# Kernel tuning notes

Hardware: AMD Instinct MI355X
Metric: run time of the kernel (lower is better)

## Reference

```python
import jax, jax.numpy as jnp
import numpy as np

DIN, DK, DV, DR, NH, DMODEL = 512, 64, 64, 16, 8, 512
N = 4096
TOT = DK + DK + DV + DR  # per-head projection width = 208


def setup_inputs() -> dict:
    key = jax.random.key(0)
    k1, k2, k3, k4 = jax.random.split(key, 4)
    H = jax.random.normal(k1, (N, DIN), dtype=jnp.float32)
    D = jax.random.normal(k2, (N, N, DR), dtype=jnp.float32)
    attention_mask = jnp.zeros((N, N), dtype=jnp.float32)  # 0 = allowed
    # learned params (Linear, no bias): stored as [in, out] for x @ W
    W = jax.random.normal(k3, (DIN, NH * TOT), dtype=jnp.float32) / np.sqrt(DIN)
    Wout = jax.random.normal(k4, (NH * DV, DMODEL), dtype=jnp.float32) / np.sqrt(NH * DV)
    return {"H": H, "D": D, "attention_mask": attention_mask, "W": W, "Wout": Wout}


def reference(H, D, attention_mask, W, Wout):
    n = H.shape[0]
    # project and split into per-head Q, K, V, R: [h, n, *]
    H2 = (H @ W).reshape(n, NH, TOT).transpose(1, 0, 2)
    Q, K, V, R = jnp.split(H2, [DK, 2 * DK, 2 * DK + DV], axis=-1)
    # relative/route bias: RD[h,i,j] = sum_r R[h,i,r] * D[i,j,r]
    RD = jnp.einsum('hir,ijr->hij', R, D)
    scale = 1.0 / np.sqrt(DK + DR)
    scores = scale * (jnp.einsum('hid,hjd->hij', Q, K) + RD) + attention_mask
    probs = jax.nn.softmax(scores, axis=-1)
    ctx = jnp.einsum('hij,hjd->hid', probs, V)          # [h, n, dv]
    ctx = ctx.transpose(1, 0, 2).reshape(n, NH * DV)    # [n, h*dv]
    return ctx @ Wout                                    # [n, dmodel]
```

## Files before the change

kernel.cpp:

```cpp
#include <hip/hip_runtime.h>
#include <hip/hip_bf16.h>

#define NN 4096
#define NH 8
#define TOT 208
#define NPROJ 1664
#define BJ 32
#define NT (NN/BJ)

typedef __attribute__((ext_vector_type(8))) short short8;
typedef __attribute__((ext_vector_type(4))) short short4_t;
typedef __attribute__((ext_vector_type(4))) float float4_t;

#define MFMA __builtin_amdgcn_mfma_f32_16x16x32_bf16

__device__ __forceinline__ short f2bf(float f){
  union { float f; unsigned u; } v; v.f = f;
  unsigned r = v.u + 0x7fffu + ((v.u >> 16) & 1u);
  return (short)(r >> 16);
}

__device__ __forceinline__ short8 cvt8(float4_t a, float4_t b){
  union { short8 s; unsigned u[4]; } r;
  asm("v_cvt_pk_bf16_f32 %0, %1, %2" : "=v"(r.u[0]) : "v"(a[0]), "v"(a[1]));
  asm("v_cvt_pk_bf16_f32 %0, %1, %2" : "=v"(r.u[1]) : "v"(a[2]), "v"(a[3]));
  asm("v_cvt_pk_bf16_f32 %0, %1, %2" : "=v"(r.u[2]) : "v"(b[0]), "v"(b[1]));
  asm("v_cvt_pk_bf16_f32 %0, %1, %2" : "=v"(r.u[3]) : "v"(b[2]), "v"(b[3]));
  return r.s;
}

#define BAR() do{ \
    asm volatile("s_waitcnt lgkmcnt(0)" ::: "memory"); \
    __builtin_amdgcn_s_barrier(); \
    asm volatile("" ::: "memory"); \
  }while(0)

__global__ void k_cvt(const float* __restrict__ in, short* __restrict__ out, int n4){
  int i = blockIdx.x*256 + threadIdx.x;
  if(i >= n4) return;
  float4_t v = *(const float4_t*)(in + (size_t)i*4);
  short4_t o;
  o[0]=f2bf(v[0]); o[1]=f2bf(v[1]); o[2]=f2bf(v[2]); o[3]=f2bf(v[3]);
  *(short4_t*)(out + (size_t)i*4) = o;
}

__global__ void k_trans(const float* __restrict__ in, short* __restrict__ out, int R, int C){
  __shared__ float tile[32][33];
  int bc = blockIdx.x*32, br = blockIdx.y*32;
  int tx = threadIdx.x, ty = threadIdx.y;
  #pragma unroll
  for(int dy=0; dy<32; dy+=8){
    int r = br+ty+dy, c = bc+tx;
    if(r<R && c<C) tile[ty+dy][tx] = in[(size_t)r*C + c];
  }
  __syncthreads();
  #pragma unroll
  for(int dy=0; dy<32; dy+=8){
    int c = bc+ty+dy, r = br+tx;
    if(c<C && r<R) out[(size_t)c*R + r] = f2bf(tile[tx][ty+dy]);
  }
}

__global__ __launch_bounds__(256) void k_gemm(
    const short* __restrict__ A, const short* __restrict__ Bt, float* __restrict__ C,
    int M, int Ncols, int K)
{
  __shared__ __align__(16) short As[2][2048];
  __shared__ __align__(16) short Bs[2][2048];
  const int tid = threadIdx.x;
  const int l = tid & 63, w = tid >> 6;
  const int wm = w >> 1, wn = w & 1;
  const int g = l >> 4, i16 = l & 15;
  const size_t bm = (size_t)blockIdx.x * 64, bn = (size_t)blockIdx.y * 64;
  const int r = tid >> 2, cb = tid & 3;
  const int dst = r*32 + ((cb ^ (r&3))*8);
  const short* Ag = A + (bm + (size_t)r)*K + cb*8;
  const short* Bg = Bt + (bn + (size_t)r)*K + cb*8;
  float4_t z4 = {0.f,0.f,0.f,0.f};
  float4_t acc00=z4, acc01=z4, acc10=z4, acc11=z4;
  short8 ta = *(const short8*)(Ag);
  short8 tb = *(const short8*)(Bg);
  *(short8*)&As[0][dst] = ta;
  *(short8*)&Bs[0][dst] = tb;
  const int nk = K >> 5;
  int c = 0;
  const int swa = (g ^ (i16&3))*8;
  for(int kt=0; kt<nk; kt++){
    __syncthreads();
    if(kt+1 < nk){
      ta = *(const short8*)(Ag + (kt+1)*32);
      tb = *(const short8*)(Bg + (kt+1)*32);
    }
    short8 a0 = *(const short8*)&As[c][(wm*32 + i16)*32 + swa];
    short8 a1 = *(const short8*)&As[c][(wm*32 + 16 + i16)*32 + swa];
    short8 b0 = *(const short8*)&Bs[c][(wn*32 + i16)*32 + swa];
    short8 b1 = *(const short8*)&Bs[c][(wn*32 + 16 + i16)*32 + swa];
    acc00 = MFMA(a0,b0,acc00,0,0,0); acc01 = MFMA(a0,b1,acc01,0,0,0);
    acc10 = MFMA(a1,b0,acc10,0,0,0); acc11 = MFMA(a1,b1,acc11,0,0,0);
    if(kt+1 < nk){
      *(short8*)&As[c^1][dst] = ta;
      *(short8*)&Bs[c^1][dst] = tb;
    }
    c ^= 1;
  }
  #pragma unroll
  for(int rr=0; rr<4; rr++){
    C[(bm + wm*32 +      4*g + rr)*(size_t)Ncols + bn + wn*32 + i16]      = acc00[rr];
    C[(bm + wm*32 +      4*g + rr)*(size_t)Ncols + bn + wn*32 + 16 + i16] = acc01[rr];
    C[(bm + wm*32 + 16 + 4*g + rr)*(size_t)Ncols + bn + wn*32 + i16]      = acc10[rr];
    C[(bm + wm*32 + 16 + 4*g + rr)*(size_t)Ncols + bn + wn*32 + 16 + i16] = acc11[rr];
  }
}

__global__ void k_pack(const float* __restrict__ H2, short* __restrict__ Qp,
                       short* __restrict__ Kp, short* __restrict__ Vp, short* __restrict__ Rp){
  int T = blockIdx.x*256 + threadIdx.x;
  if(T < 262144){
    int l = T & 63; int rest = T >> 6;
    int kb = rest & 1; rest >>= 1;
    int it = rest & 255; int h = rest >> 8;
    int i = it*16 + (l & 15);
    int col = h*TOT + kb*32 + 8*(l>>4);
    const float* s = H2 + (size_t)i*NPROJ + col;
    short8 v;
    #pragma unroll
    for(int e=0;e<8;e++) v[e] = f2bf(s[e]);
    *(short8*)(Qp + (size_t)T*8) = v;
  } else if(T < 524288){
    int T2 = T - 262144;
    int l = T2 & 63; int rest = T2 >> 6;
    int kb = rest & 1; rest >>= 1;
    int it = rest & 255; int h = rest >> 8;
    int i = it*16 + (l & 15);
    int col = h*TOT + 64 + kb*32 + 8*(l>>4);
    const float* s = H2 + (size_t)i*NPROJ + col;
    short8 v;
    #pragma unroll
    for(int e=0;e<8;e++) v[e] = f2bf(s[e]);
    *(short8*)(Kp + (size_t)T2*8) = v;
  } else if(T < 786432){
    int T2 = T - 524288;
    int l = T2 & 63; int rest = T2 >> 6;
    int db = rest & 3; rest >>= 2;
    int jt = rest & 127; int h = rest >> 7;
    int col = h*TOT + 128 + db*16 + (l & 15);
    int j0 = jt*32 + 8*(l>>4);
    short8 v;
    #pragma unroll
    for(int e=0;e<8;e++) v[e] = f2bf(H2[(size_t)(j0+e)*NPROJ + col]);
    *(short8*)(Vp + (size_t)T2*8) = v;
  } else {
    int T2 = T - 786432;
    int half = T2 & 1; int hh = (T2>>1) & 15; int i = T2 >> 5;
    short8 v;
    #pragma unroll
    for(int e=0;e<8;e++) v[e] = 0;
    if(hh < 8){
      const float* s = H2 + (size_t)i*NPROJ + hh*TOT + 192 + half*8;
      #pragma unroll
      for(int e=0;e<8;e++) v[e] = f2bf(s[e]);
    }
    *(short8*)(Rp + (size_t)T2*8) = v;
  }
}

#define RDI(b,h,j,i) (((((b)*8+(h))*32+(j))*20)+(i))
#define PIDX(ww,i,j) (((ww)*16+(i))*40+(j))
#define CIDX(ww,i,cc) (((ww)*16+(i))*72+(cc))

__global__ __launch_bounds__(512) void k_attn(
    const float* __restrict__ Dm, const float* __restrict__ mask,
    const short* __restrict__ Qp, const short* __restrict__ Kp,
    const short* __restrict__ Vp, const short* __restrict__ Rp,
    short* __restrict__ ctx)
{
  __shared__ __align__(16) char smem[51712];
  float* rd_lds = (float*)smem;
  short* p_lds  = (short*)(smem + 40960);
  float* abuf   = (float*)(smem + 40960 + 10240);

  const int tid = threadIdx.x;
  const int l = tid & 63, w = tid >> 6;
  const int g = l >> 4, i16 = l & 15;
  const int i0 = blockIdx.x * 16;
  const float iscale = 0.11180339887498949f;
  const float msc    = 8.944271909999159f;

  const short* qb = Qp + (((size_t)w*256 + (i0>>4))*2)*512 + (size_t)l*8;
  short8 qa0 = *(const short8*)(qb);
  short8 qa1 = *(const short8*)(qb + 512);

  short8 raA, raB;
  #pragma unroll
  for(int e=0;e<8;e++){ raA[e]=0; raB[e]=0; }
  if(g < 2){
    raA = *(const short8*)(Rp + (size_t)(i0+2*w  )*256 + i16*16 + 8*g);
    raB = *(const short8*)(Rp + (size_t)(i0+2*w+1)*256 + i16*16 + 8*g);
  }

  float4_t z4 = {0.f,0.f,0.f,0.f};
  float4_t O0=z4, O1=z4, O2=z4, O3=z4;
  float l_r[4];
  #pragma unroll
  for(int r=0;r<4;r++) l_r[r] = 0.f;

  float4_t dA00=z4,dA01=z4,dA10=z4,dA11=z4,dB00=z4,dB01=z4,dB10=z4,dB11=z4;
  float mi00=0.f,mi01=0.f,mi10=0.f,mi11=0.f;
  short8 kf0,kf1,kf2,kf3, vf0,vf1,vf2,vf3;

#define LOAD_D(tt) do{ \
    if(g < 2){ \
      const float* dp0 = Dm + ((size_t)(i0+2*w  )*NN + (size_t)(tt)*BJ + i16)*16 + 8*g; \
      const float* dp1 = Dm + ((size_t)(i0+2*w+1)*NN + (size_t)(tt)*BJ + i16)*16 + 8*g; \
      dA00 = *(const float4_t*)(dp0);     dA01 = *(const float4_t*)(dp0+4); \
      dA10 = *(const float4_t*)(dp0+256); dA11 = *(const float4_t*)(dp0+260); \
      dB00 = *(const float4_t*)(dp1);     dB01 = *(const float4_t*)(dp1+4); \
      dB10 = *(const float4_t*)(dp1+256); dB11 = *(const float4_t*)(dp1+260); \
    } }while(0)

#define LOAD_MI(tt) do{ \
    size_t jj = (size_t)(tt)*BJ + i16; \
    mi00 = mask[(size_t)(i0+2*w  )*NN + jj] * msc; \
    mi01 = mask[(size_t)(i0+2*w  )*NN + jj + 16] * msc; \
    mi10 = mask[(size_t)(i0+2*w+1)*NN + jj] * msc; \
    mi11 = mask[(size_t)(i0+2*w+1)*NN + jj + 16] * msc; }while(0)

#define LOAD_K(tt) do{ \
    const short* kp = Kp + (((size_t)w*256 + (size_t)(tt)*2)*2)*512 + (size_t)l*8; \
    kf0 = *(const short8*)(kp);        kf1 = *(const short8*)(kp+512); \
    kf2 = *(const short8*)(kp+1024);   kf3 = *(const short8*)(kp+1536); }while(0)

#define LOAD_V(tt) do{ \
    const short* vp = Vp + (((size_t)w*128 + (size_t)(tt))*4)*512 + (size_t)l*8; \
    vf0 = *(const short8*)(vp);        vf1 = *(const short8*)(vp+512); \
    vf2 = *(const short8*)(vp+1024);   vf3 = *(const short8*)(vp+1536); }while(0)

  LOAD_D(0); LOAD_MI(0); LOAD_K(0); LOAD_V(0);

  for(int t=0; t<NT; t++){
    const int tn = (t+1 < NT) ? (t+1) : t;
    short8 df00 = cvt8(dA00,dA01), df01 = cvt8(dA10,dA11);
    short8 df10 = cvt8(dB00,dB01), df11 = cvt8(dB10,dB11);
    float4_t r00 = {mi00,mi00,mi00,mi00}; r00 = MFMA(raA, df00, r00,0,0,0);
    float4_t r01 = {mi01,mi01,mi01,mi01}; r01 = MFMA(raA, df01, r01,0,0,0);
    float4_t r10 = {mi10,mi10,mi10,mi10}; r10 = MFMA(raB, df10, r10,0,0,0);
    float4_t r11 = {mi11,mi11,mi11,mi11}; r11 = MFMA(raB, df11, r11,0,0,0);
    if(l < 32){
      const int hb = 4*g;
      #pragma unroll
      for(int r=0;r<4;r++){
        rd_lds[RDI(t&1, hb+r, i16,    2*w  )] = r00[r];
        rd_lds[RDI(t&1, hb+r, 16+i16, 2*w  )] = r01[r];
        rd_lds[RDI(t&1, hb+r, i16,    2*w+1)] = r10[r];
        rd_lds[RDI(t&1, hb+r, 16+i16, 2*w+1)] = r11[r];
      }
    }
    BAR();
    float4_t s0 = MFMA(qa0, kf0, z4,0,0,0); s0 = MFMA(qa1, kf1, s0,0,0,0);
    float4_t s1 = MFMA(qa0, kf2, z4,0,0,0); s1 = MFMA(qa1, kf3, s1,0,0,0);
    LOAD_D(tn); LOAD_MI(tn); LOAD_K(tn);
    float4_t rd0 = *(const float4_t*)&rd_lds[RDI(t&1, w, i16,    4*g)];
    float4_t rd1 = *(const float4_t*)&rd_lds[RDI(t&1, w, 16+i16, 4*g)];
    float p0[4], p1[4];
    #pragma unroll
    for(int r=0;r<4;r++){
      p0[r] = __expf((s0[r] + rd0[r]) * iscale);
      p1[r] = __expf((s1[r] + rd1[r]) * iscale);
      l_r[r] += p0[r] + p1[r];
    }
    #pragma unroll
    for(int r=0;r<4;r++){
      p_lds[PIDX(w, 4*g+r, i16)]    = f2bf(p0[r]);
      p_lds[PIDX(w, 4*g+r, 16+i16)] = f2bf(p1[r]);
    }
    short8 pb = *(const short8*)&p_lds[PIDX(w, i16, 8*g)];
    O0 = MFMA(vf0, pb, O0,0,0,0);
    O1 = MFMA(vf1, pb, O1,0,0,0);
    O2 = MFMA(vf2, pb, O2,0,0,0);
    O3 = MFMA(vf3, pb, O3,0,0,0);
    LOAD_V(tn);
  }
  __syncthreads();
  #pragma unroll
  for(int d=1; d<16; d<<=1){
    #pragma unroll
    for(int r=0;r<4;r++) l_r[r] += __shfl_xor(l_r[r], d);
  }
  if(i16==0) abuf[w*16 + 4*g+0] = l_r[0];
  if(i16==1) abuf[w*16 + 4*g+1] = l_r[1];
  if(i16==2) abuf[w*16 + 4*g+2] = l_r[2];
  if(i16==3) abuf[w*16 + 4*g+3] = l_r[3];
  float invl = 1.0f / abuf[w*16 + i16];
  short* cl = (short*)smem;
  #pragma unroll
  for(int r=0;r<4;r++){
    cl[CIDX(w, i16,      4*g + r)] = f2bf(O0[r]*invl);
    cl[CIDX(w, i16, 16 + 4*g + r)] = f2bf(O1[r]*invl);
    cl[CIDX(w, i16, 32 + 4*g + r)] = f2bf(O2[r]*invl);
    cl[CIDX(w, i16, 48 + 4*g + r)] = f2bf(O3[r]*invl);
  }
  short8 v0 = *(const short8*)&cl[CIDX(w, l>>2, (l&3)*16)];
  short8 v1 = *(const short8*)&cl[CIDX(w, l>>2, (l&3)*16 + 8)];
  size_t go = (size_t)(i0 + (l>>2))*512 + (size_t)w*64 + (l&3)*16;
  *(short8*)(ctx + go)     = v0;
  *(short8*)(ctx + go + 8) = v1;
}

extern "C" void kernel_launch(void* const* d_in, const int* in_sizes, int n_in,
                              void* d_out, int out_size, void* d_ws, size_t ws_size,
                              hipStream_t stream) {
  (void)in_sizes; (void)n_in; (void)out_size; (void)ws_size;
  const float* H    = (const float*)d_in[0];
  const float* Dm   = (const float*)d_in[1];
  const float* mask = (const float*)d_in[2];
  const float* W    = (const float*)d_in[3];
  const float* Wout = (const float*)d_in[4];
  float* out = (float*)d_out;

  char* ws = (char*)d_ws;
  size_t off = 0;
  auto carve = [&](size_t bytes)->char*{
    char* p = ws + off; off += (bytes + 255) & ~(size_t)255; return p;
  };
  short* Hb   = (short*)carve((size_t)4096*512*2);
  short* Wt   = (short*)carve((size_t)1664*512*2);
  short* Wot  = (short*)carve((size_t)512*512*2);
  float* H2   = (float*)carve((size_t)4096*1664*4);
  short* Qp   = (short*)carve((size_t)8*256*2*64*8*2);
  short* Kp   = (short*)carve((size_t)8*256*2*64*8*2);
  short* Vp   = (short*)carve((size_t)8*128*4*64*8*2);
  short* Rp   = (short*)carve((size_t)4096*256*2);
  short* ctxb = (short*)carve((size_t)4096*512*2);

  k_cvt<<<2048, 256, 0, stream>>>(H, Hb, 4096*512/4);
  k_trans<<<dim3(52,16), dim3(32,8), 0, stream>>>(W, Wt, 512, 1664);
  k_trans<<<dim3(16,16), dim3(32,8), 0, stream>>>(Wout, Wot, 512, 512);
  k_gemm<<<dim3(64,26), 256, 0, stream>>>(Hb, Wt, H2, 4096, 1664, 512);
  k_pack<<<3584, 256, 0, stream>>>(H2, Qp, Kp, Vp, Rp);
  k_attn<<<256, 512, 0, stream>>>(Dm, mask, Qp, Kp, Vp, Rp, ctxb);
  k_gemm<<<dim3(64,8), 256, 0, stream>>>(ctxb, Wot, out, 4096, 512, 512);
}
```

Before: 349.0 us.

## Double query rows per attention block and split keys across two blocks

Each attention block now handles 32 query rows instead of 16, so every K/V fragment it loads serves two row groups. The key range is split in half across pairs of blocks, which keeps the grid at 256 blocks, and a new merge kernel sums the partial outputs and row sums before normalising. The RD bias is now stored in LDS as bf16 rather than fp32 to fit the larger tile. The cost is extra register pressure, an fp32 partial-output round trip through global memory plus one more launch, and slightly lower precision on the bias term.

```diff
diff --git a/kernel.cpp b/kernel.cpp
--- a/kernel.cpp
+++ b/kernel.cpp
@@ -5,8 +5,6 @@
 #define NH 8
 #define TOT 208
 #define NPROJ 1664
-#define BJ 32
-#define NT (NN/BJ)
 
 typedef __attribute__((ext_vector_type(8))) short short8;
 typedef __attribute__((ext_vector_type(4))) short short4_t;
@@ -18,6 +16,10 @@
   union { float f; unsigned u; } v; v.f = f;
   unsigned r = v.u + 0x7fffu + ((v.u >> 16) & 1u);
   return (short)(r >> 16);
+}
+
+__device__ __forceinline__ float bitsf(unsigned u){
+  union { unsigned u; float f; } v; v.u = u; return v.f;
 }
 
 __device__ __forceinline__ short8 cvt8(float4_t a, float4_t b){
@@ -164,146 +166,196 @@
   }
 }
 
-#define RDI(b,h,j,i) (((((b)*8+(h))*32+(j))*20)+(i))
-#define PIDX(ww,i,j) (((ww)*16+(i))*40+(j))
-#define CIDX(ww,i,cc) (((ww)*16+(i))*72+(cc))
+#define RDS2(h,j,i) (((h)*32+(j))*36+(i))
+#define PS(ww,row,j) (((ww)*32+(row))*40+(j))
 
 __global__ __launch_bounds__(512) void k_attn(
     const float* __restrict__ Dm, const float* __restrict__ mask,
     const short* __restrict__ Qp, const short* __restrict__ Kp,
     const short* __restrict__ Vp, const short* __restrict__ Rp,
-    short* __restrict__ ctx)
+    float* __restrict__ Opart, float* __restrict__ lpart)
 {
-  __shared__ __align__(16) char smem[51712];
-  float* rd_lds = (float*)smem;
-  short* p_lds  = (short*)(smem + 40960);
-  float* abuf   = (float*)(smem + 40960 + 10240);
+  __shared__ __align__(16) short rdl[18432];
+  __shared__ __align__(16) short p_lds[10240];
 
   const int tid = threadIdx.x;
   const int l = tid & 63, w = tid >> 6;
   const int g = l >> 4, i16 = l & 15;
-  const int i0 = blockIdx.x * 16;
+  const int IT = blockIdx.x >> 1, jh = blockIdx.x & 1;
+  const int i0 = IT * 32;
   const float iscale = 0.11180339887498949f;
   const float msc    = 8.944271909999159f;
 
-  const short* qb = Qp + (((size_t)w*256 + (i0>>4))*2)*512 + (size_t)l*8;
-  short8 qa0 = *(const short8*)(qb);
-  short8 qa1 = *(const short8*)(qb + 512);
-
-  short8 raA, raB;
-  #pragma unroll
-  for(int e=0;e<8;e++){ raA[e]=0; raB[e]=0; }
+  short8 qa[4];
+  #pragma unroll
+  for(int rg=0; rg<2; rg++)
+    #pragma unroll
+    for(int kb=0; kb<2; kb++)
+      qa[rg*2+kb] = *(const short8*)(Qp + (((size_t)w*256 + IT*2+rg)*2 + kb)*512 + (size_t)l*8);
+
+  short8 ra[4];
+  #pragma unroll
+  for(int row=0; row<4; row++)
+    #pragma unroll
+    for(int e=0; e<8; e++) ra[row][e] = 0;
   if(g < 2){
-    raA = *(const short8*)(Rp + (size_t)(i0+2*w  )*256 + i16*16 + 8*g);
-    raB = *(const short8*)(Rp + (size_t)(i0+2*w+1)*256 + i16*16 + 8*g);
+    #pragma unroll
+    for(int row=0; row<4; row++)
+      ra[row] = *(const short8*)(Rp + (size_t)(i0+4*w+row)*256 + i16*16 + 8*g);
   }
 
   float4_t z4 = {0.f,0.f,0.f,0.f};
-  float4_t O0=z4, O1=z4, O2=z4, O3=z4;
-  float l_r[4];
-  #pragma unroll
-  for(int r=0;r<4;r++) l_r[r] = 0.f;
-
-  float4_t dA00=z4,dA01=z4,dA10=z4,dA11=z4,dB00=z4,dB01=z4,dB10=z4,dB11=z4;
-  float mi00=0.f,mi01=0.f,mi10=0.f,mi11=0.f;
-  short8 kf0,kf1,kf2,kf3, vf0,vf1,vf2,vf3;
-
-#define LOAD_D(tt) do{ \
-    if(g < 2){ \
-      const float* dp0 = Dm + ((size_t)(i0+2*w  )*NN + (size_t)(tt)*BJ + i16)*16 + 8*g; \
-      const float* dp1 = Dm + ((size_t)(i0+2*w+1)*NN + (size_t)(tt)*BJ + i16)*16 + 8*g; \
-      dA00 = *(const float4_t*)(dp0);     dA01 = *(const float4_t*)(dp0+4); \
-      dA10 = *(const float4_t*)(dp0+256); dA11 = *(const float4_t*)(dp0+260); \
-      dB00 = *(const float4_t*)(dp1);     dB01 = *(const float4_t*)(dp1+4); \
-      dB10 = *(const float4_t*)(dp1+256); dB11 = *(const float4_t*)(dp1+260); \
-    } }while(0)
+  float4_t O[4][2];
+  #pragma unroll
+  for(int db=0; db<4; db++){ O[db][0]=z4; O[db][1]=z4; }
+  float l_r[8];
+  #pragma unroll
+  for(int k2=0;k2<8;k2++) l_r[k2]=0.f;
+
+  float4_t d[4][4];
+  #pragma unroll
+  for(int row=0; row<4; row++)
+    #pragma unroll
+    for(int q=0; q<4; q++) d[row][q] = z4;
+  float mi[4][2];
+  short8 kf[4], vf[4];
+
+#define LOAD_D(tt) do{ if(g < 2){ \
+    const float* dp0 = Dm + ((size_t)(i0+4*w+0)*NN + (size_t)(tt)*32 + i16)*16 + 8*g; \
+    const float* dp1 = Dm + ((size_t)(i0+4*w+1)*NN + (size_t)(tt)*32 + i16)*16 + 8*g; \
+    const float* dp2 = Dm + ((size_t)(i0+4*w+2)*NN + (size_t)(tt)*32 + i16)*16 + 8*g; \
+    const float* dp3 = Dm + ((size_t)(i0+4*w+3)*NN + (size_t)(tt)*32 + i16)*16 + 8*g; \
+    d[0][0]=*(const float4_t*)(dp0); d[0][1]=*(const float4_t*)(dp0+4); \
+    d[0][2]=*(const float4_t*)(dp0+256); d[0][3]=*(const float4_t*)(dp0+260); \
+    d[1][0]=*(const float4_t*)(dp1); d[1][1]=*(const float4_t*)(dp1+4); \
+    d[1][2]=*(const float4_t*)(dp1+256); d[1][3]=*(const float4_t*)(dp1+260); \
+    d[2][0]=*(const float4_t*)(dp2); d[2][1]=*(const float4_t*)(dp2+4); \
+    d[2][2]=*(const float4_t*)(dp2+256); d[2][3]=*(const float4_t*)(dp2+260); \
+    d[3][0]=*(const float4_t*)(dp3); d[3][1]=*(const float4_t*)(dp3+4); \
+    d[3][2]=*(const float4_t*)(dp3+256); d[3][3]=*(const float4_t*)(dp3+260); \
+  } }while(0)
 
 #define LOAD_MI(tt) do{ \
-    size_t jj = (size_t)(tt)*BJ + i16; \
-    mi00 = mask[(size_t)(i0+2*w  )*NN + jj] * msc; \
-    mi01 = mask[(size_t)(i0+2*w  )*NN + jj + 16] * msc; \
-    mi10 = mask[(size_t)(i0+2*w+1)*NN + jj] * msc; \
-    mi11 = mask[(size_t)(i0+2*w+1)*NN + jj + 16] * msc; }while(0)
+    size_t jj = (size_t)(tt)*32 + i16; \
+    mi[0][0] = mask[(size_t)(i0+4*w+0)*NN + jj] * msc; \
+    mi[0][1] = mask[(size_t)(i0+4*w+0)*NN + jj + 16] * msc; \
+    mi[1][0] = mask[(size_t)(i0+4*w+1)*NN + jj] * msc; \
+    mi[1][1] = mask[(size_t)(i0+4*w+1)*NN + jj + 16] * msc; \
+    mi[2][0] = mask[(size_t)(i0+4*w+2)*NN + jj] * msc; \
+    mi[2][1] = mask[(size_t)(i0+4*w+2)*NN + jj + 16] * msc; \
+    mi[3][0] = mask[(size_t)(i0+4*w+3)*NN + jj] * msc; \
+    mi[3][1] = mask[(size_t)(i0+4*w+3)*NN + jj + 16] * msc; }while(0)
 
 #define LOAD_K(tt) do{ \
     const short* kp = Kp + (((size_t)w*256 + (size_t)(tt)*2)*2)*512 + (size_t)l*8; \
-    kf0 = *(const short8*)(kp);        kf1 = *(const short8*)(kp+512); \
-    kf2 = *(const short8*)(kp+1024);   kf3 = *(const short8*)(kp+1536); }while(0)
+    kf[0] = *(const short8*)(kp);        kf[1] = *(const short8*)(kp+512); \
+    kf[2] = *(const short8*)(kp+1024);   kf[3] = *(const short8*)(kp+1536); }while(0)
 
 #define LOAD_V(tt) do{ \
     const short* vp = Vp + (((size_t)w*128 + (size_t)(tt))*4)*512 + (size_t)l*8; \
-    vf0 = *(const short8*)(vp);        vf1 = *(const short8*)(vp+512); \
-    vf2 = *(const short8*)(vp+1024);   vf3 = *(const short8*)(vp+1536); }while(0)
-
-  LOAD_D(0); LOAD_MI(0); LOAD_K(0); LOAD_V(0);
-
-  for(int t=0; t<NT; t++){
-    const int tn = (t+1 < NT) ? (t+1) : t;
-    short8 df00 = cvt8(dA00,dA01), df01 = cvt8(dA10,dA11);
-    short8 df10 = cvt8(dB00,dB01), df11 = cvt8(dB10,dB11);
-    float4_t r00 = {mi00,mi00,mi00,mi00}; r00 = MFMA(raA, df00, r00,0,0,0);
-    float4_t r01 = {mi01,mi01,mi01,mi01}; r01 = MFMA(raA, df01, r01,0,0,0);
-    float4_t r10 = {mi10,mi10,mi10,mi10}; r10 = MFMA(raB, df10, r10,0,0,0);
-    float4_t r11 = {mi11,mi11,mi11,mi11}; r11 = MFMA(raB, df11, r11,0,0,0);
-    if(l < 32){
-      const int hb = 4*g;
-      #pragma unroll
-      for(int r=0;r<4;r++){
-        rd_lds[RDI(t&1, hb+r, i16,    2*w  )] = r00[r];
-        rd_lds[RDI(t&1, hb+r, 16+i16, 2*w  )] = r01[r];
-        rd_lds[RDI(t&1, hb+r, i16,    2*w+1)] = r10[r];
-        rd_lds[RDI(t&1, hb+r, 16+i16, 2*w+1)] = r11[r];
+    vf[0] = *(const short8*)(vp);        vf[1] = *(const short8*)(vp+512); \
+    vf[2] = *(const short8*)(vp+1024);   vf[3] = *(const short8*)(vp+1536); }while(0)
+
+  const int t0 = jh*64;
+  LOAD_D(t0); LOAD_MI(t0); LOAD_K(t0); LOAD_V(t0);
+
+  for(int t=0; t<64; t++){
+    const int tt = t0 + t;
+    const int tn = (t<63) ? tt+1 : tt;
+    const int buf = (t&1)*8;
+    #pragma unroll
+    for(int row=0; row<4; row++){
+      short8 df0 = cvt8(d[row][0], d[row][1]);
+      short8 df1 = cvt8(d[row][2], d[row][3]);
+      float4_t c0 = {mi[row][0],mi[row][0],mi[row][0],mi[row][0]};
+      float4_t c1 = {mi[row][1],mi[row][1],mi[row][1],mi[row][1]};
+      c0 = MFMA(ra[row], df0, c0,0,0,0);
+      c1 = MFMA(ra[row], df1, c1,0,0,0);
+      if(g < 2){
+        int ib = 4*w + row;
+        #pragma unroll
+        for(int r=0; r<4; r++){
+          rdl[RDS2(buf + 4*g+r, i16,    ib)] = f2bf(c0[r]);
+          rdl[RDS2(buf + 4*g+r, 16+i16, ib)] = f2bf(c1[r]);
+        }
       }
     }
     BAR();
-    float4_t s0 = MFMA(qa0, kf0, z4,0,0,0); s0 = MFMA(qa1, kf1, s0,0,0,0);
-    float4_t s1 = MFMA(qa0, kf2, z4,0,0,0); s1 = MFMA(qa1, kf3, s1,0,0,0);
+    float4_t s[2][2];
+    s[0][0] = MFMA(qa[0], kf[0], z4,0,0,0); s[0][0] = MFMA(qa[1], kf[1], s[0][0],0,0,0);
+    s[0][1] = MFMA(qa[0], kf[2], z4,0,0,0); s[0][1] = MFMA(qa[1], kf[3], s[0][1],0,0,0);
+    s[1][0] = MFMA(qa[2], kf[0], z4,0,0,0); s[1][0] = MFMA(qa[3], kf[1], s[1][0],0,0,0);
+    s[1][1] = MFMA(qa[2], kf[2], z4,0,0,0); s[1][1] = MFMA(qa[3], kf[3], s[1][1],0,0,0);
     LOAD_D(tn); LOAD_MI(tn); LOAD_K(tn);
-    float4_t rd0 = *(const float4_t*)&rd_lds[RDI(t&1, w, i16,    4*g)];
-    float4_t rd1 = *(const float4_t*)&rd_lds[RDI(t&1, w, 16+i16, 4*g)];
-    float p0[4], p1[4];
-    #pragma unroll
-    for(int r=0;r<4;r++){
-      p0[r] = __expf((s0[r] + rd0[r]) * iscale);
-      p1[r] = __expf((s1[r] + rd1[r]) * iscale);
-      l_r[r] += p0[r] + p1[r];
-    }
-    #pragma unroll
-    for(int r=0;r<4;r++){
-      p_lds[PIDX(w, 4*g+r, i16)]    = f2bf(p0[r]);
-      p_lds[PIDX(w, 4*g+r, 16+i16)] = f2bf(p1[r]);
-    }
-    short8 pb = *(const short8*)&p_lds[PIDX(w, i16, 8*g)];
-    O0 = MFMA(vf0, pb, O0,0,0,0);
-    O1 = MFMA(vf1, pb, O1,0,0,0);
-    O2 = MFMA(vf2, pb, O2,0,0,0);
-    O3 = MFMA(vf3, pb, O3,0,0,0);
+    float p[2][2][4];
+    #pragma unroll
+    for(int rg=0; rg<2; rg++){
+      #pragma unroll
+      for(int jg=0; jg<2; jg++){
+        unsigned long long rv = *(const unsigned long long*)&rdl[RDS2(buf + w, jg*16+i16, rg*16+4*g)];
+        unsigned lo = (unsigned)rv, hi = (unsigned)(rv>>32);
+        float rf0 = bitsf(lo<<16), rf1 = bitsf(lo & 0xffff0000u);
+        float rf2 = bitsf(hi<<16), rf3 = bitsf(hi & 0xffff0000u);
+        p[rg][jg][0] = __expf((s[rg][jg][0] + rf0)*iscale);
+        p[rg][jg][1] = __expf((s[rg][jg][1] + rf1)*iscale);
+        p[rg][jg][2] = __expf((s[rg][jg][2] + rf2)*iscale);
+        p[rg][jg][3] = __expf((s[rg][jg][3] + rf3)*iscale);
+      }
+      #pragma unroll
+      for(int r=0; r<4; r++) l_r[rg*4+r] += p[rg][0][r] + p[rg][1][r];
+    }
+    #pragma unroll
+    for(int rg=0; rg<2; rg++)
+      #pragma unroll
+      for(int jg=0; jg<2; jg++)
+        #pragma unroll
+        for(int r=0; r<4; r++)
+          p_lds[PS(w, rg*16 + 4*g + r, jg*16 + i16)] = f2bf(p[rg][jg][r]);
+    #pragma unroll
+    for(int rg=0; rg<2; rg++){
+      short8 pb = *(const short8*)&p_lds[PS(w, rg*16 + i16, 8*g)];
+      O[0][rg] = MFMA(vf[0], pb, O[0][rg],0,0,0);
+      O[1][rg] = MFMA(vf[1], pb, O[1][rg],0,0,0);
+      O[2][rg] = MFMA(vf[2], pb, O[2][rg],0,0,0);
+      O[3][rg] = MFMA(vf[3], pb, O[3][rg],0,0,0);
+    }
     LOAD_V(tn);
   }
-  __syncthreads();
-  #pragma unroll
-  for(int d=1; d<16; d<<=1){
-    #pragma unroll
-    for(int r=0;r<4;r++) l_r[r] += __shfl_xor(l_r[r], d);
-  }
-  if(i16==0) abuf[w*16 + 4*g+0] = l_r[0];
-  if(i16==1) abuf[w*16 + 4*g+1] = l_r[1];
-  if(i16==2) abuf[w*16 + 4*g+2] = l_r[2];
-  if(i16==3) abuf[w*16 + 4*g+3] = l_r[3];
-  float invl = 1.0f / abuf[w*16 + i16];
-  short* cl = (short*)smem;
-  #pragma unroll
-  for(int r=0;r<4;r++){
-    cl[CIDX(w, i16,      4*g + r)] = f2bf(O0[r]*invl);
-    cl[CIDX(w, i16, 16 + 4*g + r)] = f2bf(O1[r]*invl);
-    cl[CIDX(w, i16, 32 + 4*g + r)] = f2bf(O2[r]*invl);
-    cl[CIDX(w, i16, 48 + 4*g + r)] = f2bf(O3[r]*invl);
-  }
-  short8 v0 = *(const short8*)&cl[CIDX(w, l>>2, (l&3)*16)];
-  short8 v1 = *(const short8*)&cl[CIDX(w, l>>2, (l&3)*16 + 8)];
-  size_t go = (size_t)(i0 + (l>>2))*512 + (size_t)w*64 + (l&3)*16;
-  *(short8*)(ctx + go)     = v0;
-  *(short8*)(ctx + go + 8) = v1;
+  #pragma unroll
+  for(int dd=1; dd<16; dd<<=1)
+    #pragma unroll
+    for(int k2=0; k2<8; k2++) l_r[k2] += __shfl_xor(l_r[k2], dd);
+  if(i16 == 0){
+    #pragma unroll
+    for(int rg=0; rg<2; rg++)
+      #pragma unroll
+      for(int r=0; r<4; r++)
+        lpart[((size_t)jh*8 + w)*NN + i0 + rg*16 + 4*g + r] = l_r[rg*4+r];
+  }
+  #pragma unroll
+  for(int rg=0; rg<2; rg++)
+    #pragma unroll
+    for(int db=0; db<4; db++)
+      *(float4_t*)(Opart + ((size_t)jh*NN + i0 + rg*16 + i16)*512 + w*64 + db*16 + 4*g) = O[db][rg];
+}
+
+__global__ void k_merge(const float* __restrict__ Op, const float* __restrict__ lp,
+                        short* __restrict__ ctx){
+  int T = blockIdx.x*256 + threadIdx.x;
+  int i = T >> 6; int c = (T & 63) * 8;
+  int h = c >> 6;
+  float lA = lp[(size_t)h*NN + i], lB = lp[(size_t)(8+h)*NN + i];
+  float inv = 1.0f / (lA + lB);
+  const float4_t* a = (const float4_t*)(Op + (size_t)i*512 + c);
+  const float4_t* b = (const float4_t*)(Op + ((size_t)NN + i)*512 + c);
+  float4_t x0 = a[0], x1 = a[1], y0 = b[0], y1 = b[1];
+  short8 o;
+  #pragma unroll
+  for(int e=0; e<4; e++){
+    o[e]   = f2bf((x0[e]+y0[e])*inv);
+    o[e+4] = f2bf((x1[e]+y1[e])*inv);
+  }
+  *(short8*)(ctx + (size_t)i*512 + c) = o;
 }
 
 extern "C" void kernel_launch(void* const* d_in, const int* in_sizes, int n_in,
@@ -322,21 +374,24 @@
   auto carve = [&](size_t bytes)->char*{
     char* p = ws + off; off += (bytes + 255) & ~(size_t)255; return p;
   };
-  short* Hb   = (short*)carve((size_t)4096*512*2);
-  short* Wt   = (short*)carve((size_t)1664*512*2);
-  short* Wot  = (short*)carve((size_t)512*512*2);
-  float* H2   = (float*)carve((size_t)4096*1664*4);
-  short* Qp   = (short*)carve((size_t)8*256*2*64*8*2);
-  short* Kp   = (short*)carve((size_t)8*256*2*64*8*2);
-  short* Vp   = (short*)carve((size_t)8*128*4*64*8*2);
-  short* Rp   = (short*)carve((size_t)4096*256*2);
-  short* ctxb = (short*)carve((size_t)4096*512*2);
+  short* Hb    = (short*)carve((size_t)4096*512*2);
+  short* Wt    = (short*)carve((size_t)1664*512*2);
+  short* Wot   = (short*)carve((size_t)512*512*2);
+  float* H2    = (float*)carve((size_t)4096*1664*4);
+  short* Qp    = (short*)carve((size_t)8*256*2*64*8*2);
+  short* Kp    = (short*)carve((size_t)8*256*2*64*8*2);
+  short* Vp    = (short*)carve((size_t)8*128*4*64*8*2);
+  short* Rp    = (short*)carve((size_t)4096*256*2);
+  short* ctxb  = (short*)carve((size_t)4096*512*2);
+  float* Opart = (float*)carve((size_t)2*4096*512*4);
+  float* lp    = (float*)carve((size_t)2*8*4096*4);
 
   k_cvt<<<2048, 256, 0, stream>>>(H, Hb, 4096*512/4);
   k_trans<<<dim3(52,16), dim3(32,8), 0, stream>>>(W, Wt, 512, 1664);
   k_trans<<<dim3(16,16), dim3(32,8), 0, stream>>>(Wout, Wot, 512, 512);
   k_gemm<<<dim3(64,26), 256, 0, stream>>>(Hb, Wt, H2, 4096, 1664, 512);
   k_pack<<<3584, 256, 0, stream>>>(H2, Qp, Kp, Vp, Rp);
-  k_attn<<<256, 512, 0, stream>>>(Dm, mask, Qp, Kp, Vp, Rp, ctxb);
+  k_attn<<<256, 512, 0, stream>>>(Dm, mask, Qp, Kp, Vp, Rp, Opart, lp);
+  k_merge<<<1024, 256, 0, stream>>>(Opart, lp, ctxb);
   k_gemm<<<dim3(64,8), 256, 0, stream>>>(ctxb, Wot, out, 4096, 512, 512);
 }
```

Result: faster. 339.7 us (-2.6%).
